# Kernel tuning notes

Measured on AMD Instinct MI355X. Metric: run time of the kernel, lower is better.

## Reference

```python
import jax, jax.numpy as jnp
import numpy as np

BS, S, DIM, H = 4, 2048, 768, 12
DH = DIM // H  # 64


def setup_inputs() -> dict:
    key = jax.random.key(0)
    ks = jax.random.split(key, 12)
    std = 0.02
    inp = {
        "query": jax.random.normal(ks[0], (BS, S, DIM), jnp.float32),
        "key_t": jax.random.normal(ks[1], (BS, S, DIM), jnp.float32),
        "value": jax.random.normal(ks[2], (BS, S, DIM), jnp.float32),
        "mask": jnp.ones((BS, S), jnp.int32),
        "q_w": jax.random.normal(ks[3], (DIM, DIM), jnp.float32) * std,
        "q_b": jnp.zeros((DIM,), jnp.float32),
        "k_w": jax.random.normal(ks[4], (DIM, DIM), jnp.float32) * std,
        "k_b": jnp.zeros((DIM,), jnp.float32),
        "v_w": jax.random.normal(ks[5], (DIM, DIM), jnp.float32) * std,
        "v_b": jnp.zeros((DIM,), jnp.float32),
        "o_w": jax.random.normal(ks[6], (DIM, DIM), jnp.float32) * std,
        "o_b": jnp.zeros((DIM,), jnp.float32),
    }
    return inp


def _shape(x, bs):
    # (bs, L, dim) -> (bs, H, L, DH)
    return x.reshape(bs, -1, H, DH).transpose(0, 2, 1, 3)


def reference(query, key_t, value, mask, q_w, q_b, k_w, k_b, v_w, v_b, o_w, o_b):
    bs, q_len, _ = query.shape
    k_len = key_t.shape[1]
    q = _shape(query @ q_w.T + q_b, bs)   # (bs,H,Sq,DH)
    k = _shape(key_t @ k_w.T + k_b, bs)   # (bs,H,Sk,DH)
    v = _shape(value @ v_w.T + v_b, bs)
    q = q * (1.0 / jnp.sqrt(jnp.asarray(DH, q.dtype)))
    scores = jnp.einsum("bhqd,bhkd->bhqk", q, k)  # (bs,H,Sq,Sk)
    pad = (mask == 0)[:, None, None, :]           # (bs,1,1,Sk)
    neg = jnp.finfo(scores.dtype).min
    scores = jnp.where(pad, neg, scores)
    weights = jax.nn.softmax(scores, axis=-1)
    context = jnp.einsum("bhqk,bhkd->bhqd", weights, v)
    context = context.transpose(0, 2, 1, 3).reshape(bs, q_len, H * DH)
    out = context @ o_w.T + o_b
    return out
```

## Files before the change

### kernel.cpp

```cpp
#include <hip/hip_runtime.h>


#define BSZ 4
#define SEQ 2048
#define DIMD 768
#define NHD 12
#define MTOT (BSZ*SEQ)
#define WELEM (DIMD*DIMD)

typedef __bf16 bf16;
typedef __attribute__((ext_vector_type(8))) __bf16 bf16x8;
typedef __attribute__((ext_vector_type(4))) __bf16 bf16x4;
typedef __attribute__((ext_vector_type(4))) float f32x4;

__device__ __forceinline__ f32x4 mfma_bf16(bf16x8 a, bf16x8 b, f32x4 c) {
    return __builtin_amdgcn_mfma_f32_16x16x32_bf16(a, b, c, 0, 0, 0);
}

__device__ __forceinline__ void async16(const bf16* g, bf16* l) {
    __builtin_amdgcn_global_load_lds(
        (const __attribute__((address_space(1))) unsigned int*)g,
        (__attribute__((address_space(3))) unsigned int*)l, 16, 0, 0);
}

__global__ __launch_bounds__(256) void convert_all_kernel(
    const float* __restrict__ w0, const float* __restrict__ w1,
    const float* __restrict__ w2, const float* __restrict__ w3,
    const float* __restrict__ x0, const float* __restrict__ x1,
    const float* __restrict__ x2,
    bf16* __restrict__ W, bf16* __restrict__ d0, bf16* __restrict__ d1,
    bf16* __restrict__ d2) {
    int id = blockIdx.x;
    const float* src;
    bf16* dst;
    int base;
    if (id < 2304) {
        const int z = id / 576, r = id - z * 576;
        src = (z == 0) ? w0 : (z == 1) ? w1 : (z == 2) ? w2 : w3;
        dst = W + (size_t)z * WELEM;
        base = r * 1024;
    } else {
        id -= 2304;
        const int z = id / 6144, r = id - z * 6144;
        src = (z == 0) ? x0 : (z == 1) ? x1 : x2;
        dst = (z == 0) ? d0 : (z == 1) ? d1 : d2;
        base = r * 1024;
    }
    const int i = base + threadIdx.x * 4;
    float4 v = *(const float4*)(src + i);
    bf16x4 o;
    o[0] = (bf16)v.x; o[1] = (bf16)v.y; o[2] = (bf16)v.z; o[3] = (bf16)v.w;
    *(bf16x4*)(dst + i) = o;
}

__device__ __forceinline__ void gemm_core_768(
    const bf16* __restrict__ Ag, const bf16* __restrict__ Bg,
    int m0, int n0, bf16* As, bf16* Bs, f32x4 (&acc)[4][4]) {
    const int tid = threadIdx.x;
    const int lane = tid & 63, wv = tid >> 6;
    const int quad = lane >> 4, l16 = lane & 15;
    const int wr = wv >> 1, wc = wv & 1;
    const int rr = lane >> 3, cbl = lane & 7;
    const int swz = l16 & 7;
    for (int kt = 0; kt < 12; ++kt) {
        if (kt) __syncthreads();
        for (int c = 0; c < 4; ++c) {
            const int row = c * 32 + wv * 8 + rr;
            const int cb = cbl ^ (row & 7);
            const size_t gcol = (size_t)kt * 64 + cb * 8;
            async16(Ag + (size_t)(m0 + row) * 768 + gcol, As + row * 64 + cbl * 8);
            async16(Bg + (size_t)(n0 + row) * 768 + gcol, Bs + row * 64 + cbl * 8);
        }
        __syncthreads();
        for (int ks = 0; ks < 2; ++ks) {
            bf16x8 af[4], bfr[4];
            for (int t = 0; t < 4; ++t)
                af[t] = *(const bf16x8*)(As + (wr * 64 + t * 16 + l16) * 64 +
                                         (((ks * 4 + quad) ^ swz) * 8));
            for (int t = 0; t < 4; ++t)
                bfr[t] = *(const bf16x8*)(Bs + (wc * 64 + t * 16 + l16) * 64 +
                                          (((ks * 4 + quad) ^ swz) * 8));
            for (int ti = 0; ti < 4; ++ti)
                for (int tj = 0; tj < 4; ++tj)
                    acc[ti][tj] = mfma_bf16(af[ti], bfr[tj], acc[ti][tj]);
        }
    }
}

__global__ __launch_bounds__(256, 3) void proj_kernel(
    const bf16* __restrict__ Xq, const bf16* __restrict__ Xk, const bf16* __restrict__ Xv,
    const bf16* __restrict__ W,
    const float* __restrict__ bq, const float* __restrict__ bk, const float* __restrict__ bv,
    bf16* __restrict__ Qo, bf16* __restrict__ Ko, bf16* __restrict__ Vo) {
    __shared__ __align__(16) bf16 smem[2 * 128 * 64];
    bf16* As = smem;
    bf16* Bs = smem + 128 * 64;
    const int lin = blockIdx.x;
    const int swzb = (lin & 7) * 144 + (lin >> 3);
    const int z = swzb / 384;
    const int rem = swzb - z * 384;
    const int rt = rem / 6;
    const int xt = rem - rt * 6;
    const bf16* X = (z == 0) ? Xq : (z == 1) ? Xk : Xv;
    const bf16* Wz = W + (size_t)z * WELEM;
    const float* bias = (z == 0) ? bq : (z == 1) ? bk : bv;
    bf16* Out = (z == 0) ? Qo : (z == 1) ? Ko : Vo;

    const int tid = threadIdx.x;
    const int lane = tid & 63, wv = tid >> 6;
    const int quad = lane >> 4, l16 = lane & 15;
    const int wr = wv >> 1, wc = wv & 1;
    f32x4 acc[4][4] = {};
    int m0, n0;
    const bf16 *Ag, *Bg;
    if (z < 2) { m0 = xt * 128; n0 = rt * 128; Ag = Wz; Bg = X; }
    else       { m0 = rt * 128; n0 = xt * 128; Ag = X;  Bg = Wz; }
    gemm_core_768(Ag, Bg, m0, n0, As, Bs, acc);
    __syncthreads();
    bf16* Ot = smem;
    if (z < 2) {
        const float scale = (z == 0) ? 0.18033688011112042f : 1.0f;
        for (int ti = 0; ti < 4; ++ti) {
            const int featl = wr * 64 + ti * 16 + quad * 4;
            const float4 b4 = *(const float4*)(bias + m0 + featl);
            for (int tj = 0; tj < 4; ++tj) {
                const int sl = wc * 64 + tj * 16 + l16;
                bf16x4 pk;
                pk[0] = (bf16)((acc[ti][tj][0] + b4.x) * scale);
                pk[1] = (bf16)((acc[ti][tj][1] + b4.y) * scale);
                pk[2] = (bf16)((acc[ti][tj][2] + b4.z) * scale);
                pk[3] = (bf16)((acc[ti][tj][3] + b4.w) * scale);
                *(bf16x4*)&Ot[sl * 128 + featl] = pk;
            }
        }
        __syncthreads();
        for (int it = 0; it < 8; ++it) {
            const int unit = it * 256 + tid;
            const int s = unit >> 4, u = unit & 15;
            const int feat = m0 + u * 8;
            const int hh = feat >> 6, dh = feat & 63;
            const int srow = n0 + s;
            const int bb = srow >> 11, s2 = srow & 2047;
            *(bf16x8*)&Out[((size_t)(bb * NHD + hh) * SEQ + s2) * 64 + dh] =
                *(const bf16x8*)&Ot[s * 128 + u * 8];
        }
    } else {
        for (int ti = 0; ti < 4; ++ti) {
            const int sl = wr * 64 + ti * 16 + quad * 4;
            for (int tj = 0; tj < 4; ++tj) {
                const int featl = wc * 64 + tj * 16 + l16;
                const float bv = bias[n0 + featl];
                bf16x4 pk;
                pk[0] = (bf16)(acc[ti][tj][0] + bv);
                pk[1] = (bf16)(acc[ti][tj][1] + bv);
                pk[2] = (bf16)(acc[ti][tj][2] + bv);
                pk[3] = (bf16)(acc[ti][tj][3] + bv);
                *(bf16x4*)&Ot[featl * 128 + sl] = pk;
            }
        }
        __syncthreads();
        const int bb = m0 >> 11, sbase = m0 & 2047;
        for (int it = 0; it < 8; ++it) {
            const int unit = it * 256 + tid;
            const int fl = unit >> 4, u = unit & 15;
            const int feat = n0 + fl;
            const int hh = feat >> 6, dh = feat & 63;
            *(bf16x8*)&Out[((size_t)(bb * NHD + hh) * 64 + dh) * SEQ + sbase + u * 8] =
                *(const bf16x8*)&Ot[fl * 128 + u * 8];
        }
    }
}

__global__ __launch_bounds__(256, 3) void attn_kernel(
    const bf16* __restrict__ Qb, const bf16* __restrict__ Kb, const bf16* __restrict__ Vb,
    const int* __restrict__ mask, bf16* __restrict__ CTX) {
    __shared__ __align__(16) bf16 Ps[2][128][64];
    __shared__ __align__(16) bf16 Ks[2][64][64];
    __shared__ float alphas[2][128];
    __shared__ float invs[128];
    __shared__ int anyz_s;
    const int tid = threadIdx.x;
    const int lane = tid & 63, wv = tid >> 6, quad = lane >> 4, l16 = lane & 15;
    const int swz = l16 & 7;
    const int lin = blockIdx.x;
    const int nb = (lin & 7) * 96 + (lin >> 3);
    const int qt = nb & 15;
    const int bh = nb >> 4;
    const int b = bh / NHD, h = bh - b * NHD;
    if (tid == 0) anyz_s = 0;
    __syncthreads();
    {
        int4 m0v = *(const int4*)(mask + b * SEQ + tid * 8);
        int4 m1v = *(const int4*)(mask + b * SEQ + tid * 8 + 4);
        if (!(m0v.x && m0v.y && m0v.z && m0v.w && m1v.x && m1v.y && m1v.z && m1v.w))
            anyz_s = 1;
    }
    bf16x8 qf0[2], qf1[2];
    for (int st = 0; st < 2; ++st) {
        const bf16* qp = Qb + ((size_t)bh * SEQ + qt * 128 + wv * 32 + st * 16 + l16) * 64;
        qf0[st] = *(const bf16x8*)(qp + quad * 8);
        qf1[st] = *(const bf16x8*)(qp + 32 + quad * 8);
    }
    const bf16* Kg = Kb + (size_t)bh * SEQ * 64;
    const bf16* Vp = Vb + (size_t)bh * 64 * SEQ + (size_t)(wv * 16 + l16) * SEQ + quad * 8;
    const int* Mp = mask + b * SEQ;
    f32x4 acc_o[8] = {};
    float rm[2] = {-1e30f, -1e30f}, rs[2] = {0.f, 0.f};

    const int s_sub = lane >> 3;
    const int s_row = wv * 8 + s_sub;
    const int s_dst = (lane & 7) * 8;
    const int s_src = ((lane & 7) ^ s_sub) * 8;
#define STAGE_K(BUF, K0) do {                                                  \
        async16(Kg + (size_t)((K0) + s_row) * 64 + s_src,                      \
                &Ks[BUF][s_row][s_dst]);                                       \
        async16(Kg + (size_t)((K0) + 32 + s_row) * 64 + s_src,                 \
                &Ks[BUF][32 + s_row][s_dst]);                                  \
    } while (0)

    STAGE_K(0, 0);
    __syncthreads();
    const int az = anyz_s;

    for (int kt = 0; kt < SEQ / 64; ++kt) {
        const int cur = kt & 1, nxt = cur ^ 1, k0 = kt * 64;
        const int kn = (kt < SEQ / 64 - 1) ? k0 + 64 : k0;
        STAGE_K(nxt, kn);
        bf16x8 vf0 = *(const bf16x8*)(Vp + k0);
        bf16x8 vf1 = *(const bf16x8*)(Vp + k0 + 32);
        bf16x8 kf0[4], kf1[4];
        #pragma unroll
        for (int jj = 0; jj < 4; ++jj) {
            const bf16* kr = &Ks[cur][jj * 16 + l16][0];
            kf0[jj] = *(const bf16x8*)(kr + ((quad ^ swz) * 8));
            kf1[jj] = *(const bf16x8*)(kr + (((4 + quad) ^ swz) * 8));
        }
        #pragma unroll
        for (int st = 0; st < 2; ++st) {
            f32x4 sc[4];
            #pragma unroll
            for (int jj = 0; jj < 4; ++jj) {
                f32x4 zf = {};
                zf = mfma_bf16(kf0[jj], qf0[st], zf);
                sc[jj] = mfma_bf16(kf1[jj], qf1[st], zf);
            }
            if (az) {
                #pragma unroll
                for (int jj = 0; jj < 4; ++jj) {
                    const int4 mm = *(const int4*)(Mp + k0 + jj * 16 + quad * 4);
                    sc[jj][0] += mm.x ? 0.f : -1e30f;
                    sc[jj][1] += mm.y ? 0.f : -1e30f;
                    sc[jj][2] += mm.z ? 0.f : -1e30f;
                    sc[jj][3] += mm.w ? 0.f : -1e30f;
                }
            }
            float tmax = -1e30f;
            #pragma unroll
            for (int jj = 0; jj < 4; ++jj)
                #pragma unroll
                for (int r = 0; r < 4; ++r) tmax = fmaxf(tmax, sc[jj][r]);
            tmax = fmaxf(tmax, __shfl_xor(tmax, 16));
            tmax = fmaxf(tmax, __shfl_xor(tmax, 32));
            const float nmax = fmaxf(rm[st], tmax);
            const float alpha = exp2f(rm[st] - nmax);
            rm[st] = nmax;
            float tsum = 0.f;
            bf16* prow = &Ps[cur][wv * 32 + st * 16 + l16][0];
            #pragma unroll
            for (int jj = 0; jj < 4; ++jj) {
                bf16x4 pk;
                #pragma unroll
                for (int r = 0; r < 4; ++r) {
                    const float p = exp2f(sc[jj][r] - nmax);
                    tsum += p;
                    pk[r] = (bf16)p;
                }
                *(bf16x4*)&prow[(jj * 16 + quad * 4) ^ (swz * 8)] = pk;
            }
            tsum += __shfl_xor(tsum, 16);
            tsum += __shfl_xor(tsum, 32);
            rs[st] = rs[st] * alpha + tsum;
            if (lane < 16) alphas[cur][wv * 32 + st * 16 + lane] = alpha;
        }
        __syncthreads();
        #pragma unroll
        for (int qj = 0; qj < 8; ++qj) {
            const float al = alphas[cur][qj * 16 + l16];
            f32x4 c = acc_o[qj];
            c[0] *= al; c[1] *= al; c[2] *= al; c[3] *= al;
            const bf16* pr = &Ps[cur][qj * 16 + l16][0];
            bf16x8 pf0 = *(const bf16x8*)(pr + ((quad ^ swz) * 8));
            bf16x8 pf1 = *(const bf16x8*)(pr + (((4 + quad) ^ swz) * 8));
            c = mfma_bf16(vf0, pf0, c);
            c = mfma_bf16(vf1, pf1, c);
            acc_o[qj] = c;
        }
    }
#undef STAGE_K

    if (lane < 16) {
        invs[wv * 32 + lane] = 1.0f / rs[0];
        invs[wv * 32 + 16 + lane] = 1.0f / rs[1];
    }
    __syncthreads();
    for (int qj = 0; qj < 8; ++qj) {
        const float inv = invs[qj * 16 + l16];
        bf16x4 pk;
        for (int r = 0; r < 4; ++r) pk[r] = (bf16)(acc_o[qj][r] * inv);
        const int s = qt * 128 + qj * 16 + l16;
        *(bf16x4*)&CTX[(size_t)(b * SEQ + s) * DIMD + h * 64 + wv * 16 + quad * 4] = pk;
    }
}

__global__ __launch_bounds__(256, 3) void oproj_kernel(
    const bf16* __restrict__ ctx, const bf16* __restrict__ wo,
    const float* __restrict__ bo, float* __restrict__ out) {
    __shared__ __align__(16) bf16 smem[2 * 128 * 64];
    const int lin = blockIdx.x;
    const int swzb = (lin & 7) * 48 + (lin >> 3);
    const int rt = swzb / 6;
    const int xt = swzb - rt * 6;
    const int tid = threadIdx.x;
    const int lane = tid & 63, wv = tid >> 6;
    const int quad = lane >> 4, l16 = lane & 15;
    const int wr = wv >> 1, wc = wv & 1;
    const int m0 = rt * 128, n0 = xt * 128;
    f32x4 acc[4][4] = {};
    gemm_core_768(ctx, wo, m0, n0, smem, smem + 128 * 64, acc);
    for (int ti = 0; ti < 4; ++ti) {
        const int rowb = m0 + wr * 64 + ti * 16 + quad * 4;
        for (int tj = 0; tj < 4; ++tj) {
            const int feat = n0 + wc * 64 + tj * 16 + l16;
            const float bv = bo[feat];
            for (int r = 0; r < 4; ++r)
                out[(size_t)(rowb + r) * DIMD + feat] = acc[ti][tj][r] + bv;
        }
    }
}

extern "C" void kernel_launch(void* const* d_in, const int* in_sizes, int n_in,
                              void* d_out, int out_size, void* d_ws, size_t ws_size,
                              hipStream_t stream) {
    const float* query = (const float*)d_in[0];
    const float* key_t = (const float*)d_in[1];
    const float* value = (const float*)d_in[2];
    const int*   mask  = (const int*)d_in[3];
    const float* q_w = (const float*)d_in[4];
    const float* q_b = (const float*)d_in[5];
    const float* k_w = (const float*)d_in[6];
    const float* k_b = (const float*)d_in[7];
    const float* v_w = (const float*)d_in[8];
    const float* v_b = (const float*)d_in[9];
    const float* o_w = (const float*)d_in[10];
    const float* o_b = (const float*)d_in[11];
    float* out = (float*)d_out;

    bf16* ws  = (bf16*)d_ws;
    bf16* W   = ws;
    bf16* XBq = ws + (size_t)4 * WELEM;
    bf16* XBk = XBq + (size_t)MTOT * DIMD;
    bf16* XBv = XBk + (size_t)MTOT * DIMD;
    bf16* Qb  = XBv + (size_t)MTOT * DIMD;
    bf16* Kb  = Qb + (size_t)MTOT * DIMD;
    bf16* Vb  = Kb + (size_t)MTOT * DIMD;
    bf16* CTX = XBq;

    convert_all_kernel<<<2304 + 3 * 6144, 256, 0, stream>>>(
        q_w, k_w, v_w, o_w, query, key_t, value, W, XBq, XBk, XBv);

    proj_kernel<<<1152, 256, 0, stream>>>(XBq, XBk, XBv, W, q_b, k_b, v_b, Qb, Kb, Vb);

    attn_kernel<<<768, 256, 0, stream>>>(Qb, Kb, Vb, mask, CTX);
    oproj_kernel<<<384, 256, 0, stream>>>(CTX, W + (size_t)3 * WELEM, o_b, out);
}
```

Measured before the change: 293.0 us.

## Make each wave own its query rows for PV and stage V through LDS

The attention kernel previously split the PV product by head-dim column across waves, which forced all waves to share the P tile and per-row alphas through LDS and a barrier. Now each wave computes the output for its own 32 query rows over all 64 head dims, keeping P in a per-wave LDS slice. V is staged asynchronously into LDS alongside K with double buffering instead of being read from global memory per lane. A lazy rescale skips the alpha correction unless some row max grows by more than a threshold, which trades extra accumulator registers and a small rounding-range risk for fewer exp and multiply operations.

```diff
diff --git a/kernel.cpp b/kernel.cpp
--- a/kernel.cpp
+++ b/kernel.cpp
@@ -174,10 +174,9 @@
 __global__ __launch_bounds__(256, 3) void attn_kernel(
     const bf16* __restrict__ Qb, const bf16* __restrict__ Kb, const bf16* __restrict__ Vb,
     const int* __restrict__ mask, bf16* __restrict__ CTX) {
-    __shared__ __align__(16) bf16 Ps[2][128][64];
     __shared__ __align__(16) bf16 Ks[2][64][64];
-    __shared__ float alphas[2][128];
-    __shared__ float invs[128];
+    __shared__ __align__(16) bf16 Vs[2][64][64];
+    __shared__ __align__(16) bf16 Ps[4][32][64];
     __shared__ int anyz_s;
     const int tid = threadIdx.x;
     const int lane = tid & 63, wv = tid >> 6, quad = lane >> 4, l16 = lane & 15;
@@ -202,32 +201,35 @@
         qf1[st] = *(const bf16x8*)(qp + 32 + quad * 8);
     }
     const bf16* Kg = Kb + (size_t)bh * SEQ * 64;
-    const bf16* Vp = Vb + (size_t)bh * 64 * SEQ + (size_t)(wv * 16 + l16) * SEQ + quad * 8;
+    const bf16* Vg = Vb + (size_t)bh * 64 * SEQ;
     const int* Mp = mask + b * SEQ;
-    f32x4 acc_o[8] = {};
+    bf16* Pw = &Ps[wv][0][0];
+    f32x4 acc[2][4] = {};
     float rm[2] = {-1e30f, -1e30f}, rs[2] = {0.f, 0.f};
 
     const int s_sub = lane >> 3;
     const int s_row = wv * 8 + s_sub;
     const int s_dst = (lane & 7) * 8;
     const int s_src = ((lane & 7) ^ s_sub) * 8;
-#define STAGE_K(BUF, K0) do {                                                  \
+#define STAGE_KV(BUF, K0) do {                                                 \
         async16(Kg + (size_t)((K0) + s_row) * 64 + s_src,                      \
                 &Ks[BUF][s_row][s_dst]);                                       \
         async16(Kg + (size_t)((K0) + 32 + s_row) * 64 + s_src,                 \
                 &Ks[BUF][32 + s_row][s_dst]);                                  \
+        async16(Vg + (size_t)s_row * SEQ + (K0) + s_src,                       \
+                &Vs[BUF][s_row][s_dst]);                                       \
+        async16(Vg + (size_t)(32 + s_row) * SEQ + (K0) + s_src,                \
+                &Vs[BUF][32 + s_row][s_dst]);                                  \
     } while (0)
 
-    STAGE_K(0, 0);
+    STAGE_KV(0, 0);
     __syncthreads();
     const int az = anyz_s;
 
     for (int kt = 0; kt < SEQ / 64; ++kt) {
-        const int cur = kt & 1, nxt = cur ^ 1, k0 = kt * 64;
+        const int cur = kt & 1, k0 = kt * 64;
         const int kn = (kt < SEQ / 64 - 1) ? k0 + 64 : k0;
-        STAGE_K(nxt, kn);
-        bf16x8 vf0 = *(const bf16x8*)(Vp + k0);
-        bf16x8 vf1 = *(const bf16x8*)(Vp + k0 + 32);
+        STAGE_KV(cur ^ 1, kn);
         bf16x8 kf0[4], kf1[4];
         #pragma unroll
         for (int jj = 0; jj < 4; ++jj) {
@@ -261,54 +263,71 @@
                 for (int r = 0; r < 4; ++r) tmax = fmaxf(tmax, sc[jj][r]);
             tmax = fmaxf(tmax, __shfl_xor(tmax, 16));
             tmax = fmaxf(tmax, __shfl_xor(tmax, 32));
-            const float nmax = fmaxf(rm[st], tmax);
-            const float alpha = exp2f(rm[st] - nmax);
-            rm[st] = nmax;
+            if (__any(tmax > rm[st] + 8.0f)) {
+                const float nmax = fmaxf(rm[st], tmax);
+                const float alpha = exp2f(rm[st] - nmax);
+                rm[st] = nmax;
+                rs[st] *= alpha;
+                #pragma unroll
+                for (int d = 0; d < 4; ++d) {
+                    acc[st][d][0] *= alpha; acc[st][d][1] *= alpha;
+                    acc[st][d][2] *= alpha; acc[st][d][3] *= alpha;
+                }
+            }
             float tsum = 0.f;
-            bf16* prow = &Ps[cur][wv * 32 + st * 16 + l16][0];
+            const float m = rm[st];
             #pragma unroll
             for (int jj = 0; jj < 4; ++jj) {
                 bf16x4 pk;
                 #pragma unroll
                 for (int r = 0; r < 4; ++r) {
-                    const float p = exp2f(sc[jj][r] - nmax);
+                    const float p = exp2f(sc[jj][r] - m);
                     tsum += p;
                     pk[r] = (bf16)p;
                 }
-                *(bf16x4*)&prow[(jj * 16 + quad * 4) ^ (swz * 8)] = pk;
+                *(bf16x4*)&Pw[(st * 16 + l16) * 64 + ((jj * 16 + quad * 4) ^ (swz * 8))] = pk;
             }
             tsum += __shfl_xor(tsum, 16);
             tsum += __shfl_xor(tsum, 32);
-            rs[st] = rs[st] * alpha + tsum;
-            if (lane < 16) alphas[cur][wv * 32 + st * 16 + lane] = alpha;
-        }
+            rs[st] += tsum;
+        }
+        bf16x8 vf[4][2];
+        #pragma unroll
+        for (int d = 0; d < 4; ++d) {
+            const bf16* vr = &Vs[cur][d * 16 + l16][0];
+            #pragma unroll
+            for (int kb = 0; kb < 2; ++kb)
+                vf[d][kb] = *(const bf16x8*)(vr + (((kb * 4 + quad) ^ swz) * 8));
+        }
+        bf16x8 pf[2][2];
+        #pragma unroll
+        for (int st = 0; st < 2; ++st)
+            #pragma unroll
+            for (int kb = 0; kb < 2; ++kb)
+                pf[st][kb] = *(const bf16x8*)&Pw[(st * 16 + l16) * 64 +
+                                                (((kb * 4 + quad) ^ swz) * 8)];
+        #pragma unroll
+        for (int st = 0; st < 2; ++st)
+            #pragma unroll
+            for (int kb = 0; kb < 2; ++kb)
+                #pragma unroll
+                for (int d = 0; d < 4; ++d)
+                    acc[st][d] = mfma_bf16(vf[d][kb], pf[st][kb], acc[st][d]);
         __syncthreads();
-        #pragma unroll
-        for (int qj = 0; qj < 8; ++qj) {
-            const float al = alphas[cur][qj * 16 + l16];
-            f32x4 c = acc_o[qj];
-            c[0] *= al; c[1] *= al; c[2] *= al; c[3] *= al;
-            const bf16* pr = &Ps[cur][qj * 16 + l16][0];
-            bf16x8 pf0 = *(const bf16x8*)(pr + ((quad ^ swz) * 8));
-            bf16x8 pf1 = *(const bf16x8*)(pr + (((4 + quad) ^ swz) * 8));
-            c = mfma_bf16(vf0, pf0, c);
-            c = mfma_bf16(vf1, pf1, c);
-            acc_o[qj] = c;
-        }
-    }
-#undef STAGE_K
-
-    if (lane < 16) {
-        invs[wv * 32 + lane] = 1.0f / rs[0];
-        invs[wv * 32 + 16 + lane] = 1.0f / rs[1];
-    }
-    __syncthreads();
-    for (int qj = 0; qj < 8; ++qj) {
-        const float inv = invs[qj * 16 + l16];
-        bf16x4 pk;
-        for (int r = 0; r < 4; ++r) pk[r] = (bf16)(acc_o[qj][r] * inv);
-        const int s = qt * 128 + qj * 16 + l16;
-        *(bf16x4*)&CTX[(size_t)(b * SEQ + s) * DIMD + h * 64 + wv * 16 + quad * 4] = pk;
+    }
+#undef STAGE_KV
+
+    #pragma unroll
+    for (int st = 0; st < 2; ++st) {
+        const float inv = 1.0f / rs[st];
+        const int s = qt * 128 + wv * 32 + st * 16 + l16;
+        #pragma unroll
+        for (int d = 0; d < 4; ++d) {
+            bf16x4 pk;
+            #pragma unroll
+            for (int r = 0; r < 4; ++r) pk[r] = (bf16)(acc[st][d][r] * inv);
+            *(bf16x4*)&CTX[(size_t)(b * SEQ + s) * DIMD + h * 64 + d * 16 + quad * 4] = pk;
+        }
     }
 }
 
```

Result: no change. 298.9 us (+2.0%).
